# Performance work log

Measured on AMD Instinct MI355X. Metric: run time of the kernel, lower is better.

## Reference

```python
import jax, jax.numpy as jnp
import numpy as np

H = 4    # heads
D = 64   # embed_dim


def setup_inputs() -> dict:
    key = jax.random.key(0)
    ks = jax.random.split(key, 10)
    N, L = 128, 1024
    f = jnp.float32
    return {
        "seq_items": jax.random.normal(ks[0], (N, L, D), f),
        "target_items": jax.random.normal(ks[1], (N, D), f),
        "memory": jax.random.normal(ks[2], (N, D), f),
        # nn.Linear weights stored torch-style [out_features, in_features]
        "Wk": jax.random.normal(ks[3], (H * D, D), f) * 0.1,
        "Wq": jax.random.normal(ks[4], (H * D, D), f) * 0.1,
        "Wv": jax.random.normal(ks[5], (H * D, D), f) * 0.1,
        "Wu": jax.random.normal(ks[6], (D, H * D), f) * 0.1,
        "bu": jnp.zeros((D,), f),
        "W1": jax.random.normal(ks[7], (8, 4 * D), f) * 0.1,
        "b1": jnp.zeros((8,), f),
        "W2": jax.random.normal(ks[8], (1, 8), f) * 0.1,
        "b2": jnp.zeros((1,), f),
    }


def reference(seq_items, target_items, memory, Wk, Wq, Wv, Wu, bu, W1, b1, W2, b2):
    N, L, d = seq_items.shape
    # projections, split into heads: [N, L, H, D]
    e = (seq_items @ Wk.T).reshape(N, L, H, D)
    V = (seq_items @ Wv.T).reshape(N, L, H, D)
    v = (target_items @ Wq.T).reshape(N, 1, H, D)   # broadcast over L
    m = memory.reshape(N, 1, 1, D)                   # broadcast over L and heads
    # np.where(e_, 1, 0): 1 where nonzero
    mask = (e != 0).astype(e.dtype)
    a1 = (v - e) * mask
    a2 = (v * e) * mask
    a3 = (m - e) * mask
    a4 = (m * e) * mask
    alpha = jnp.concatenate([a1, a2, a3, a4], axis=-1)  # [N, L, H, 4D]
    # tiny MLP attention scorer: 4D -> 8 -> 1, sigmoid each
    hmid = jax.nn.sigmoid(alpha @ W1.T + b1)
    att = jax.nn.sigmoid(hmid @ W2.T + b2)              # [N, L, H, 1]
    out = jnp.einsum('nlhq,nlhd->nqhd', att, V).reshape(N, H * D)
    output = out @ Wu.T + bu                            # [N, D]
    return output, att
```

## Files before the change

### kernel.cpp

```cpp
#include <hip/hip_runtime.h>
#include <math.h>

#define NN 128
#define LL 1024
#define HH 4
#define DD 64
#define NCHUNK 8
#define CROWS 128

#define WS_ZT  0
#define WS_C   16384
#define WS_WTB 20480

typedef __attribute__((ext_vector_type(8))) short short8;
typedef __attribute__((ext_vector_type(4))) float f32x4;

__device__ __forceinline__ float sigm(float x) {
    return __builtin_amdgcn_rcpf(1.f + __expf(-x));
}

__device__ __forceinline__ unsigned short f2bf(float x) {
    union { float f; unsigned u; } v; v.f = x;
    unsigned r = v.u + 0x7FFFu + ((v.u >> 16) & 1u);
    return (unsigned short)(r >> 16);
}

__device__ __forceinline__ short8 pack_bf8(float4 a, float4 b) {
    short8 r;
    r[0] = (short)f2bf(a.x); r[1] = (short)f2bf(a.y);
    r[2] = (short)f2bf(a.z); r[3] = (short)f2bf(a.w);
    r[4] = (short)f2bf(b.x); r[5] = (short)f2bf(b.y);
    r[6] = (short)f2bf(b.z); r[7] = (short)f2bf(b.w);
    return r;
}

__global__ void __launch_bounds__(256) precompute_kernel(
    const float* __restrict__ target, const float* __restrict__ memv,
    const float* __restrict__ Wk, const float* __restrict__ Wq,
    const float* __restrict__ Wv, const float* __restrict__ Wu,
    const float* __restrict__ W1, const float* __restrict__ b1,
    const float* __restrict__ bu,
    unsigned short* __restrict__ Wtb, float* __restrict__ cvg,
    float* __restrict__ Zt, float* __restrict__ out)
{
    const int b = blockIdx.x;
    const int t = threadIdx.x;

    if (b < 32) {
        const int idx = b * 256 + t;
        out[idx] = bu[idx & 63];
        return;
    }
    if (b < 96) {
        const int q = b - 32;
        const int h = t >> 6, k = t & 63;
        float s = 0.f;
        #pragma unroll 8
        for (int d = 0; d < 64; ++d)
            s = fmaf(Wu[q * 256 + h * 64 + d], Wv[(h * 64 + d) * 64 + k], s);
        Zt[t * 64 + q] = s;
        return;
    }

    const int nh = b - 96;
    const int n = nh >> 2, h = nh & 3;

    __shared__ __align__(16) float tl[64];
    __shared__ __align__(16) float ml[64];
    __shared__ float vh[64];
    __shared__ float wh[64 * 8];
    __shared__ float cp[64];

    if (t < 64)       tl[t] = target[n * 64 + t];
    else if (t < 128) ml[t - 64] = memv[n * 64 + (t - 64)];
    __syncthreads();

    {
        const int d = t >> 2, kq = t & 3;
        const float4* wq4 = reinterpret_cast<const float4*>(Wq + (h * 64 + d) * 64 + kq * 16);
        const float4* tl4 = reinterpret_cast<const float4*>(tl + kq * 16);
        float s = 0.f;
        #pragma unroll
        for (int c = 0; c < 4; ++c) {
            const float4 a = wq4[c], bb = tl4[c];
            s = fmaf(a.x, bb.x, s); s = fmaf(a.y, bb.y, s);
            s = fmaf(a.z, bb.z, s); s = fmaf(a.w, bb.w, s);
        }
        s += __shfl_xor(s, 1);
        s += __shfl_xor(s, 2);
        if (kq == 0) vh[d] = s;
    }
    __syncthreads();

    {
        const int d = t & 63, jh = t >> 6;
        const float vv = vh[d], mm = ml[d];
        #pragma unroll
        for (int r = 0; r < 2; ++r) {
            const int j = jh + r * 4;
            float wv = -W1[j * 256 + d] - W1[j * 256 + 128 + d];
            wv = fmaf(W1[j * 256 + 64 + d], vv, wv);
            wv = fmaf(W1[j * 256 + 192 + d], mm, wv);
            wh[d * 8 + j] = wv;
        }
    }
    if (t < 64) {
        const int j = t >> 3, sl = t & 7;
        float s = 0.f;
        #pragma unroll
        for (int d8 = 0; d8 < 8; ++d8) {
            const int d = sl * 8 + d8;
            s = fmaf(W1[j * 256 + d], vh[d], s);
            s = fmaf(W1[j * 256 + 128 + d], ml[d], s);
        }
        cp[t] = s;
    }
    __syncthreads();
    if (t < 8) {
        float s = b1[t];
        #pragma unroll
        for (int sl = 0; sl < 8; ++sl) s += cp[t * 8 + sl];
        cvg[n * 32 + h * 8 + t] = s;
    }

    {
        const int k = t & 63, jp = t >> 6;
        float s0 = 0.f, s1 = 0.f;
        #pragma unroll 8
        for (int d = 0; d < 64; ++d) {
            const float wk = Wk[(h * 64 + d) * 64 + k];
            s0 = fmaf(wk, wh[d * 8 + jp], s0);
            s1 = fmaf(wk, wh[d * 8 + jp + 4], s1);
        }
        unsigned short* dst = Wtb + ((size_t)n * 32 + h * 8) * 64;
        dst[jp * 64 + k]       = f2bf(s0);
        dst[(jp + 4) * 64 + k] = f2bf(s1);
    }
}

__global__ void __launch_bounds__(256, 4) main_kernel(
    const float* __restrict__ seq, const unsigned short* __restrict__ Wtb,
    const float* __restrict__ cvg, const float* __restrict__ W2,
    const float* __restrict__ b2, const float* __restrict__ Zt,
    float* __restrict__ att_out, float* __restrict__ out)
{
    const int n = blockIdx.x >> 3;
    const int chunk = blockIdx.x & 7;
    const int l0 = chunk * CROWS;
    const int t = threadIdx.x;
    const int lane = t & 63;
    const int w = t >> 6;

    __shared__ __align__(16) short seq_bf[128 * 72];
    __shared__ __align__(16) short wt_lds[32 * 72];
    __shared__ float cvl[32];
    __shared__ __align__(16) float att_l[512];
    __shared__ __align__(16) float Tp_l[4][256];
    __shared__ float T_l[256];
    __shared__ float op[256];

    const float* sbase = seq + ((size_t)n * LL + l0) * 64;

    #pragma unroll
    for (int g = 0; g < 4; ++g) {
        const int p4 = g * 256 + t;
        const int l = p4 >> 3, seg = p4 & 7;
        const float* rp = sbase + l * 64 + seg * 8;
        const float4 a = *reinterpret_cast<const float4*>(rp);
        const float4 bb = *reinterpret_cast<const float4*>(rp + 4);
        *reinterpret_cast<short8*>(seq_bf + l * 72 + seg * 8) = pack_bf8(a, bb);
    }
    {
        const int row = t >> 3, seg = t & 7;
        const int4 wv = *reinterpret_cast<const int4*>(
            Wtb + ((size_t)n * 32 + row) * 64 + seg * 8);
        *reinterpret_cast<int4*>(wt_lds + row * 72 + seg * 8) = wv;
    }
    if (t < 32) cvl[t] = cvg[n * 32 + t];
    __syncthreads();

    const int rt = w & 1;
    const int ctbase = (w >> 1) * 4;
    const int g = lane >> 4;
    const int cidx = lane & 15;

    short8 afrag[2];
    #pragma unroll
    for (int ks = 0; ks < 2; ++ks)
        afrag[ks] = *reinterpret_cast<const short8*>(
            wt_lds + (rt * 16 + cidx) * 72 + ks * 32 + g * 8);

    f32x4 acc[4];
    #pragma unroll
    for (int ct = 0; ct < 4; ++ct)
        #pragma unroll
        for (int r = 0; r < 4; ++r)
            acc[ct][r] = cvl[rt * 16 + g * 4 + r];

    #pragma unroll
    for (int ct = 0; ct < 4; ++ct) {
        const int l = (ctbase + ct) * 16 + cidx;
        const short8 bf0 = *reinterpret_cast<const short8*>(seq_bf + l * 72 + g * 8);
        const short8 bf1 = *reinterpret_cast<const short8*>(seq_bf + l * 72 + 32 + g * 8);
        acc[ct] = __builtin_amdgcn_mfma_f32_16x16x32_bf16(afrag[0], bf0, acc[ct], 0, 0, 0);
        acc[ct] = __builtin_amdgcn_mfma_f32_16x16x32_bf16(afrag[1], bf1, acc[ct], 0, 0, 0);
    }

    {
        const float4 w2v = *reinterpret_cast<const float4*>(W2 + 4 * (g & 1));
        const float b2v = b2[0];
        #pragma unroll
        for (int ct = 0; ct < 4; ++ct) {
            float local = w2v.x * sigm(acc[ct][0]);
            local = fmaf(w2v.y, sigm(acc[ct][1]), local);
            local = fmaf(w2v.z, sigm(acc[ct][2]), local);
            local = fmaf(w2v.w, sigm(acc[ct][3]), local);
            local += __shfl_xor(local, 16);
            const float attv = sigm(b2v + local);
            if ((lane & 16) == 0) {
                const int l = (ctbase + ct) * 16 + cidx;
                const int h = 2 * rt + (g >> 1);
                att_l[l * 4 + h] = attv;
            }
        }
    }
    __syncthreads();

    {
        float* dst = att_out + ((size_t)n * LL + l0) * 4;
        dst[t] = att_l[t];
        dst[256 + t] = att_l[256 + t];
    }

    {
        float th0 = 0.f, th1 = 0.f, th2 = 0.f, th3 = 0.f;
        const float* sq = sbase + (w * 32) * 64 + lane;
        #pragma unroll 4
        for (int li = 0; li < 32; ++li) {
            const float s = sq[li * 64];
            const float4 a = *reinterpret_cast<const float4*>(att_l + (w * 32 + li) * 4);
            th0 = fmaf(a.x, s, th0); th1 = fmaf(a.y, s, th1);
            th2 = fmaf(a.z, s, th2); th3 = fmaf(a.w, s, th3);
        }
        Tp_l[w][0 * 64 + lane] = th0;
        Tp_l[w][1 * 64 + lane] = th1;
        Tp_l[w][2 * 64 + lane] = th2;
        Tp_l[w][3 * 64 + lane] = th3;
    }
    __syncthreads();

    T_l[t] = Tp_l[0][t] + Tp_l[1][t] + Tp_l[2][t] + Tp_l[3][t];
    __syncthreads();

    {
        const int q = t & 63, wq = t >> 6;
        float s = 0.f;
        #pragma unroll 8
        for (int i = 0; i < 64; ++i) {
            const int p = wq * 64 + i;
            s = fmaf(T_l[p], Zt[p * 64 + q], s);
        }
        op[t] = s;
    }
    __syncthreads();
    if (t < 64) {
        const float s = op[t] + op[64 + t] + op[128 + t] + op[192 + t];
        atomicAdd(out + n * 64 + t, s);
    }
}

extern "C" void kernel_launch(void* const* d_in, const int* in_sizes, int n_in,
                              void* d_out, int out_size, void* d_ws, size_t ws_size,
                              hipStream_t stream) {
    const float* seq    = (const float*)d_in[0];
    const float* target = (const float*)d_in[1];
    const float* memv   = (const float*)d_in[2];
    const float* Wk     = (const float*)d_in[3];
    const float* Wq     = (const float*)d_in[4];
    const float* Wv     = (const float*)d_in[5];
    const float* Wu     = (const float*)d_in[6];
    const float* bu     = (const float*)d_in[7];
    const float* W1     = (const float*)d_in[8];
    const float* b1     = (const float*)d_in[9];
    const float* W2     = (const float*)d_in[10];
    const float* b2     = (const float*)d_in[11];

    float* out = (float*)d_out;
    float* att = out + NN * DD;

    float* ws  = (float*)d_ws;
    float* Ztw = ws + WS_ZT;
    float* cvg = ws + WS_C;
    unsigned short* Wtb = (unsigned short*)(ws + WS_WTB);

    precompute_kernel<<<608, 256, 0, stream>>>(target, memv, Wk, Wq, Wv, Wu, W1, b1,
                                               bu, Wtb, cvg, Ztw, out);
    main_kernel<<<NN * NCHUNK, 256, 0, stream>>>(seq, Wtb, cvg, W2, b2, Ztw,
                                                 att, out);
}
```

Measured before the change: 22.31 us.

## Stage Wk in LDS, reuse bf16 seq tile, raise occupancy, use HIP bf16 conversion

The precompute kernel now stages each head's Wk slice into LDS instead of reading it repeatedly from global memory. The main kernel's attention-weighted sum over seq reads the bf16 copy already in LDS rather than re-reading fp32 seq from global memory. That lowers precision of the V-side accumulation to bf16 inputs. Launch bounds are raised to 5 blocks per CU, and the manual float-to-bf16 rounding is replaced by the HIP intrinsic.

Result: faster. 21.86 us (-2.0%).

```diff
diff --git a/kernel.cpp b/kernel.cpp
--- a/kernel.cpp
+++ b/kernel.cpp
@@ -1,4 +1,5 @@
 #include <hip/hip_runtime.h>
+#include <hip/hip_bf16.h>
 #include <math.h>
 
 #define NN 128
@@ -19,18 +20,16 @@
     return __builtin_amdgcn_rcpf(1.f + __expf(-x));
 }
 
-__device__ __forceinline__ unsigned short f2bf(float x) {
-    union { float f; unsigned u; } v; v.f = x;
-    unsigned r = v.u + 0x7FFFu + ((v.u >> 16) & 1u);
-    return (unsigned short)(r >> 16);
+__device__ __forceinline__ short bf16s(float x) {
+    __hip_bfloat16 h = __float2bfloat16(x);
+    union { __hip_bfloat16 hh; short s; } u; u.hh = h;
+    return u.s;
 }
 
 __device__ __forceinline__ short8 pack_bf8(float4 a, float4 b) {
     short8 r;
-    r[0] = (short)f2bf(a.x); r[1] = (short)f2bf(a.y);
-    r[2] = (short)f2bf(a.z); r[3] = (short)f2bf(a.w);
-    r[4] = (short)f2bf(b.x); r[5] = (short)f2bf(b.y);
-    r[6] = (short)f2bf(b.z); r[7] = (short)f2bf(b.w);
+    r[0] = bf16s(a.x); r[1] = bf16s(a.y); r[2] = bf16s(a.z); r[3] = bf16s(a.w);
+    r[4] = bf16s(b.x); r[5] = bf16s(b.y); r[6] = bf16s(b.z); r[7] = bf16s(b.w);
     return r;
 }
 
@@ -70,9 +69,18 @@
     __shared__ float vh[64];
     __shared__ float wh[64 * 8];
     __shared__ float cp[64];
+    __shared__ __align__(16) float wk_lds[64 * 64];
 
     if (t < 64)       tl[t] = target[n * 64 + t];
     else if (t < 128) ml[t - 64] = memv[n * 64 + (t - 64)];
+
+    {
+        const float4* src = reinterpret_cast<const float4*>(Wk + h * 4096);
+        float4* dst = reinterpret_cast<float4*>(wk_lds);
+        #pragma unroll
+        for (int i = 0; i < 4; ++i)
+            dst[i * 256 + t] = src[i * 256 + t];
+    }
     __syncthreads();
 
     {
@@ -128,17 +136,17 @@
         float s0 = 0.f, s1 = 0.f;
         #pragma unroll 8
         for (int d = 0; d < 64; ++d) {
-            const float wk = Wk[(h * 64 + d) * 64 + k];
+            const float wk = wk_lds[d * 64 + k];
             s0 = fmaf(wk, wh[d * 8 + jp], s0);
             s1 = fmaf(wk, wh[d * 8 + jp + 4], s1);
         }
         unsigned short* dst = Wtb + ((size_t)n * 32 + h * 8) * 64;
-        dst[jp * 64 + k]       = f2bf(s0);
-        dst[(jp + 4) * 64 + k] = f2bf(s1);
-    }
-}
-
-__global__ void __launch_bounds__(256, 4) main_kernel(
+        dst[jp * 64 + k]       = (unsigned short)bf16s(s0);
+        dst[(jp + 4) * 64 + k] = (unsigned short)bf16s(s1);
+    }
+}
+
+__global__ void __launch_bounds__(256, 5) main_kernel(
     const float* __restrict__ seq, const unsigned short* __restrict__ Wtb,
     const float* __restrict__ cvg, const float* __restrict__ W2,
     const float* __restrict__ b2, const float* __restrict__ Zt,
@@ -234,11 +242,12 @@
 
     {
         float th0 = 0.f, th1 = 0.f, th2 = 0.f, th3 = 0.f;
-        const float* sq = sbase + (w * 32) * 64 + lane;
         #pragma unroll 4
         for (int li = 0; li < 32; ++li) {
-            const float s = sq[li * 64];
-            const float4 a = *reinterpret_cast<const float4*>(att_l + (w * 32 + li) * 4);
+            const int l = w * 32 + li;
+            const float s = __uint_as_float(
+                ((unsigned)(unsigned short)seq_bf[l * 72 + lane]) << 16);
+            const float4 a = *reinterpret_cast<const float4*>(att_l + l * 4);
             th0 = fmaf(a.x, s, th0); th1 = fmaf(a.y, s, th1);
             th2 = fmaf(a.z, s, th2); th3 = fmaf(a.w, s, th3);
         }
```
